# Optimization experiments

Measured on AMD Instinct MI355X. Metric: run time of the kernel, lower is better.

The kernel has to match this reference:

```python
import jax, jax.numpy as jnp
import numpy as np

P = 2; NH = 8; NW = 4; NB = 6; D = 512; HID = 2048; NREG = 1; T = 1000; NACT = 3
HH = 32; WW = 32; C = 3; B = 1; DUR = 6


def _kron_bool(a, b):
    # kron(A,B)[i*p+k, j*q+l] = A[i,j] & B[k,l]
    m, n = a.shape; p, q = b.shape
    return (a[:, None, :, None] & b[None, :, None, :]).reshape(m * p, n * q)


def _masks(dur_zr, seq_zr, dur_xa, seq_xa):
    m_left = _kron_bool(jnp.eye(dur_zr, dtype=bool), jnp.ones((seq_zr, seq_zr), dtype=bool))
    tmp = jnp.ones((dur_zr, dur_zr), dtype=bool)
    band = jnp.tril(tmp, -1) ^ jnp.tril(tmp, -1 - NW)  # sliding window over previous frames
    m_right = _kron_bool(band[:, :-1], jnp.ones((seq_zr, seq_xa), dtype=bool))
    m_self = _kron_bool(jnp.tril(jnp.ones((dur_xa, dur_xa), dtype=bool)), jnp.ones((seq_xa, seq_xa), dtype=bool))
    return ~jnp.concatenate([m_left, m_right], axis=1), ~m_self


def _ln(x):
    mu = jnp.mean(x, -1, keepdims=True)
    xc = x - mu
    var = jnp.mean(xc * xc, -1, keepdims=True)
    return xc * jax.lax.rsqrt(var + 1e-5)


def _patch(x, Wp, bp):
    b, dur, c, h, w = x.shape
    x = x.reshape(b, dur, c, h // P, P, w // P, P)
    x = x.transpose(0, 1, 3, 5, 2, 4, 6).reshape(b, dur, (h // P) * (w // P), c * P * P)
    return x @ Wp + bp


def _unpatch(x, Wu, bu):
    b, dur, s, d = x.shape
    y = x @ Wu + bu  # [b,dur,s,C*P*P]
    y = y.reshape(b, dur, HH // P, WW // P, C, P, P)
    return y.transpose(0, 1, 4, 2, 5, 3, 6).reshape(b, dur, C, HH, WW)


def _mod(x, cond, Wm, bm):
    # AdaLN: per-frame scale/shift broadcast over tokens of that frame
    scale, shift = jnp.split(jax.nn.silu(cond) @ Wm + bm, 2, axis=-1)
    b, L, d = x.shape; dur = cond.shape[1]; s = L // dur
    y = _ln(x).reshape(b, dur, s, d)
    return (y * (1.0 + scale[:, :, None]) + shift[:, :, None]).reshape(b, L, d)


def _gate(x, cond, Wg, bg):
    g = cond @ Wg + bg
    b, L, d = x.shape; dur = cond.shape[1]; s = L // dur
    return (x.reshape(b, dur, s, d) * g[:, :, None]).reshape(b, L, d)


def _attn(q, kv, mask, Wq, bq, Wk, bk, Wv, bv, Wo, bo):
    b, lq, d = q.shape; lk = kv.shape[1]; dh = d // NH
    qh = (q @ Wq + bq).reshape(b, lq, NH, dh)
    kh = (kv @ Wk + bk).reshape(b, lk, NH, dh)
    vh = (kv @ Wv + bv).reshape(b, lk, NH, dh)
    s = jnp.einsum('bqhd,bkhd->bhqk', qh, kh) * (1.0 / np.sqrt(dh))
    s = jnp.where(mask[None, None], -1e9, s)  # mask True = disallowed
    o = jnp.einsum('bhqk,bkhd->bqhd', jax.nn.softmax(s, axis=-1), vh)
    return o.reshape(b, lq, d) @ Wo + bo


def _geglu(x, Wg, bg, Wo, bo):
    a, g = jnp.split(x @ Wg + bg, 2, axis=-1)
    return (a * jax.nn.gelu(g, approximate=False)) @ Wo + bo


def _forward(z, frames, actions, ts, W_patch, b_patch, W_unpatch, b_unpatch, registers, pe_grid, action_emb, time_emb, W_mod1, b_mod1, W_mod2, b_mod2, W_q, b_q, W_k, b_k, W_v, b_v, W_o, b_o, W_g1, b_g1, W_g2, b_g2, W_geglu, b_geglu, W_ffout, b_ffout):
    zt = _patch(z, W_patch, b_patch) + pe_grid[None, None]
    xt = _patch(frames, W_patch, b_patch) + pe_grid[None, None]
    a = action_emb[actions]  # [B, dur, D]
    b, dur_zr, s, d = zt.shape
    zr = jnp.concatenate([zt, jnp.broadcast_to(registers[None, None], (b, dur_zr, NREG, d))], axis=2)
    xa = jnp.concatenate([xt, a[:, :-1, None, :]], axis=2)
    seq_zr = zr.shape[2]; dur_xa = xa.shape[1]; seq_xa = xa.shape[2]
    mask_cross, mask_self = _masks(dur_zr, seq_zr, dur_xa, seq_xa)
    zr = zr.reshape(b, dur_zr * seq_zr, d)
    xa = xa.reshape(b, dur_xa * seq_xa, d)
    cond = time_emb[ts]  # [B, dur_zr, D]
    clean = jnp.broadcast_to(time_emb[0][None, None], (b, dur_xa, d))
    for i in range(NB):
        zrn = _mod(zr, cond, W_mod1[i], b_mod1[i])
        xan = _mod(xa, clean, W_mod1[i], b_mod1[i])
        xkv = jnp.concatenate([zrn, xan], axis=1)
        cross = _attn(zrn, xkv, mask_cross, W_q[i], b_q[i], W_k[i], b_k[i], W_v[i], b_v[i], W_o[i], b_o[i])
        selfa = _attn(xan, xan, mask_self, W_q[i], b_q[i], W_k[i], b_k[i], W_v[i], b_v[i], W_o[i], b_o[i])
        zr = _gate(zrn, cond, W_g1[i], b_g1[i])
        xa = _gate(xan, clean, W_g1[i], b_g1[i])
        zr = _mod(zr + cross, cond, W_mod2[i], b_mod2[i])
        xa = _mod(xa + selfa, clean, W_mod2[i], b_mod2[i])
        zr = _geglu(zr, W_geglu[i], b_geglu[i], W_ffout[i], b_ffout[i])
        xa = _geglu(xa, W_geglu[i], b_geglu[i], W_ffout[i], b_ffout[i])
        zr = _gate(zr, cond, W_g2[i], b_g2[i])
        xa = _gate(xa, clean, W_g2[i], b_g2[i])
    zr = zr.reshape(b, dur_zr, seq_zr, d)[:, :, :-NREG]
    return _unpatch(zr, W_unpatch, b_unpatch)


def setup_inputs() -> dict:
    key = jax.random.key(0)
    ks = iter(jax.random.split(key, 64))
    def rn(shape, scale=0.02):
        return jax.random.normal(next(ks), shape, dtype=jnp.float32) * scale
    inp = {}
    inp['z'] = jax.random.normal(next(ks), (B, DUR, C, HH, WW), dtype=jnp.float32)
    inp['frames'] = jax.random.normal(next(ks), (B, DUR - 1, C, HH, WW), dtype=jnp.float32)
    inp['actions'] = jax.random.randint(next(ks), (B, DUR), 0, NACT)
    inp['ts'] = jax.random.randint(next(ks), (B, DUR), 0, T)
    inp['W_patch'] = rn((C * P * P, D)); inp['b_patch'] = jnp.zeros((D,), jnp.float32)
    inp['W_unpatch'] = rn((D, C * P * P)); inp['b_unpatch'] = jnp.zeros((C * P * P,), jnp.float32)
    inp['registers'] = rn((NREG, D), 1.0 / D ** 0.5)
    inp['pe_grid'] = rn(((HH // P) * (WW // P), D), 1.0 / D ** 0.5)
    inp['action_emb'] = rn((NACT, D), 1.0)
    inp['time_emb'] = rn((T, D), 1.0)
    inp['W_mod1'] = rn((NB, D, 2 * D)); inp['b_mod1'] = jnp.zeros((NB, 2 * D), jnp.float32)
    inp['W_mod2'] = rn((NB, D, 2 * D)); inp['b_mod2'] = jnp.zeros((NB, 2 * D), jnp.float32)
    for nm in ('q', 'k', 'v', 'o'):
        inp['W_' + nm] = rn((NB, D, D)); inp['b_' + nm] = jnp.zeros((NB, D), jnp.float32)
    inp['W_g1'] = rn((NB, D, D)); inp['b_g1'] = jnp.ones((NB, D), jnp.float32)
    inp['W_g2'] = rn((NB, D, D)); inp['b_g2'] = jnp.ones((NB, D), jnp.float32)
    inp['W_geglu'] = rn((NB, D, 2 * HID)); inp['b_geglu'] = jnp.zeros((NB, 2 * HID), jnp.float32)
    inp['W_ffout'] = rn((NB, HID, D)); inp['b_ffout'] = jnp.zeros((NB, D), jnp.float32)
    return inp


def reference(z, frames, actions, ts, W_patch, b_patch, W_unpatch, b_unpatch, registers, pe_grid, action_emb, time_emb, W_mod1, b_mod1, W_mod2, b_mod2, W_q, b_q, W_k, b_k, W_v, b_v, W_o, b_o, W_g1, b_g1, W_g2, b_g2, W_geglu, b_geglu, W_ffout, b_ffout):
    return _forward(z, frames, actions, ts, W_patch, b_patch, W_unpatch, b_unpatch, registers, pe_grid, action_emb, time_emb, W_mod1, b_mod1, W_mod2, b_mod2, W_q, b_q, W_k, b_k, W_v, b_v, W_o, b_o, W_g1, b_g1, W_g2, b_g2, W_geglu, b_geglu, W_ffout, b_ffout)
```

## Files before the change

kernel.cpp:

```cpp
#include <hip/hip_runtime.h>
#include <hip/hip_bf16.h>
#include <math.h>

#define DURZ 6
#define DURX 5
#define SEQ 257
#define LZ 1542
#define LX 1285
#define LT 2827
#define LTP 2880
#define DM 512
#define NHEADS 8
#define DH 64
#define HIDDEN 2048

typedef __bf16 bf16x8 __attribute__((ext_vector_type(8)));
typedef __bf16 bf16x4 __attribute__((ext_vector_type(4)));
typedef float f32x4 __attribute__((ext_vector_type(4)));

__global__ void fill_kernel(float* __restrict__ out, int n, float v) {
    int i = blockIdx.x * blockDim.x + threadIdx.x;
    if (i < n) out[i] = v;
}

__global__ void embed_kernel(const float* __restrict__ z,
                             const float* __restrict__ frames,
                             const int* __restrict__ actions,
                             const float* __restrict__ W_patch,
                             const float* __restrict__ b_patch,
                             const float* __restrict__ registers,
                             const float* __restrict__ pe,
                             const float* __restrict__ action_emb,
                             float* __restrict__ state) {
    int T = blockIdx.x;
    int tid = threadIdx.x;
    bool is_z = T < LZ;
    int T2 = is_z ? T : T - LZ;
    int f = T2 / SEQ, t = T2 % SEQ;
    if (t < 256) {
        const float* src = is_z ? z : frames;
        int hp = t >> 4, wp = t & 15;
        float pv[12];
#pragma unroll
        for (int c = 0; c < 3; c++)
#pragma unroll
            for (int ph = 0; ph < 2; ph++)
#pragma unroll
                for (int pw = 0; pw < 2; pw++)
                    pv[c * 4 + ph * 2 + pw] =
                        src[((f * 3 + c) * 32 + (hp * 2 + ph)) * 32 + (wp * 2 + pw)];
        for (int d = tid; d < DM; d += 256) {
            float acc = b_patch[d];
#pragma unroll
            for (int j = 0; j < 12; j++) acc += pv[j] * W_patch[j * DM + d];
            acc += pe[t * DM + d];
            state[T * DM + d] = acc;
        }
    } else if (is_z) {
        for (int d = tid; d < DM; d += 256) state[T * DM + d] = registers[d];
    } else {
        int a = actions[f];
        for (int d = tid; d < DM; d += 256) state[T * DM + d] = action_emb[a * DM + d];
    }
}

__global__ void cond_kernel(const int* __restrict__ ts,
                            const float* __restrict__ time_emb,
                            float* __restrict__ condraw,
                            float* __restrict__ condsilu) {
    int idx = blockIdx.x * blockDim.x + threadIdx.x;
    if (idx >= 7 * 512) return;
    int r = idx >> 9;
    int j = idx & 511;
    int tsr = (r < 6) ? ts[r] : 0;
    float x = time_emb[tsr * 512 + j];
    condraw[idx] = x;
    condsilu[idx] = x / (1.0f + expf(-x));
}

__global__ void params_kernel(const float* __restrict__ condraw,
                              const float* __restrict__ condsilu,
                              const float* __restrict__ W_mod1,
                              const float* __restrict__ b_mod1,
                              const float* __restrict__ W_mod2,
                              const float* __restrict__ b_mod2,
                              const float* __restrict__ W_g1,
                              const float* __restrict__ b_g1,
                              const float* __restrict__ W_g2,
                              const float* __restrict__ b_g2,
                              float* __restrict__ params) {
    int idx = blockIdx.x * blockDim.x + threadIdx.x;
    if (idx >= 6 * 7 * 3072) return;
    int i = idx / 21504;
    int rem = idx % 21504;
    int r = rem / 3072;
    int c = rem % 3072;
    const float* cv;
    const float* W;
    float bias;
    int ldw;
    if (c < 1024) {
        cv = condsilu + r * 512;
        W = W_mod1 + (size_t)i * 512 * 1024 + c; ldw = 1024;
        bias = b_mod1[i * 1024 + c];
    } else if (c < 2048) {
        int cc = c - 1024;
        cv = condsilu + r * 512;
        W = W_mod2 + (size_t)i * 512 * 1024 + cc; ldw = 1024;
        bias = b_mod2[i * 1024 + cc];
    } else if (c < 2560) {
        int cc = c - 2048;
        cv = condraw + r * 512;
        W = W_g1 + (size_t)i * 512 * 512 + cc; ldw = 512;
        bias = b_g1[i * 512 + cc];
    } else {
        int cc = c - 2560;
        cv = condraw + r * 512;
        W = W_g2 + (size_t)i * 512 * 512 + cc; ldw = 512;
        bias = b_g2[i * 512 + cc];
    }
    float acc = bias;
    for (int j = 0; j < 512; j++) acc += cv[j] * W[(size_t)j * ldw];
    params[idx] = acc;
}

__global__ void ztail_kernel(__bf16* __restrict__ Kh, __bf16* __restrict__ Kl,
                             __bf16* __restrict__ Vth, __bf16* __restrict__ Vtl) {
    int idx = blockIdx.x * blockDim.x + threadIdx.x;
    if (idx >= (LTP - LT) * 512) return;
    int r = idx / 512, c = idx % 512;
    Kh[(size_t)(LT + r) * DM + c] = (__bf16)0.0f;
    Kl[(size_t)(LT + r) * DM + c] = (__bf16)0.0f;
    Vth[(size_t)c * LTP + LT + r] = (__bf16)0.0f;
    Vtl[(size_t)c * LTP + LT + r] = (__bf16)0.0f;
}

template<bool PL>
__global__ __launch_bounds__(256) void lnmod_kernel(const float* __restrict__ xf,
                                                    const __bf16* __restrict__ xh,
                                                    const __bf16* __restrict__ xl,
                                                    __bf16* __restrict__ yh,
                                                    __bf16* __restrict__ yl,
                                                    const float* __restrict__ params,
                                                    int mod_off) {
    int T = blockIdx.x;
    int tid = threadIdx.x;
    int r = (T < LZ) ? (T / SEQ) : 6;
    const float* prow = params + r * 3072 + mod_off;
    size_t base = (size_t)T * DM;
    float v0, v1;
    if constexpr (PL) {
        v0 = (float)xh[base + tid] + (float)xl[base + tid];
        v1 = (float)xh[base + tid + 256] + (float)xl[base + tid + 256];
    } else {
        v0 = xf[base + tid];
        v1 = xf[base + tid + 256];
    }
    float s_ = v0 + v1, q_ = v0 * v0 + v1 * v1;
#pragma unroll
    for (int off = 32; off; off >>= 1) {
        s_ += __shfl_down(s_, off);
        q_ += __shfl_down(q_, off);
    }
    __shared__ float sh[8];
    int wave = tid >> 6, lane = tid & 63;
    if (lane == 0) { sh[wave] = s_; sh[4 + wave] = q_; }
    __syncthreads();
    float sum = sh[0] + sh[1] + sh[2] + sh[3];
    float sq = sh[4] + sh[5] + sh[6] + sh[7];
    float mu = sum * (1.0f / 512.0f);
    float var = sq * (1.0f / 512.0f) - mu * mu;
    float rstd = rsqrtf(var + 1e-5f);
    float y0 = (v0 - mu) * rstd * (1.0f + prow[tid]) + prow[512 + tid];
    float y1 = (v1 - mu) * rstd * (1.0f + prow[tid + 256]) + prow[512 + tid + 256];
    __bf16 h0 = (__bf16)y0, h1 = (__bf16)y1;
    yh[base + tid] = h0;
    yl[base + tid] = (__bf16)(y0 - (float)h0);
    yh[base + tid + 256] = h1;
    yl[base + tid + 256] = (__bf16)(y1 - (float)h1);
}

#define MFMA3(accv, ah, al, bh, bl)                                            \
    accv = __builtin_amdgcn_mfma_f32_16x16x32_bf16(al, bh, accv, 0, 0, 0);     \
    accv = __builtin_amdgcn_mfma_f32_16x16x32_bf16(ah, bl, accv, 0, 0, 0);     \
    accv = __builtin_amdgcn_mfma_f32_16x16x32_bf16(ah, bh, accv, 0, 0, 0);

__global__ __launch_bounds__(256) void wprep_kernel(const float* __restrict__ Wq,
                                                    const float* __restrict__ Wk,
                                                    const float* __restrict__ Wv,
                                                    const float* __restrict__ Wo,
                                                    const float* __restrict__ Wglu,
                                                    const float* __restrict__ Wff,
                                                    float* __restrict__ Wp) {
    __shared__ __align__(16) __bf16 T[2][64][40];
    int id = blockIdx.x, t = threadIdx.x;
    const float* src;
    int N, nsub, kt;
    size_t dstf;
    if (id < 512) {
        int mat = id >> 7, rem = id & 127;
        nsub = rem >> 4; kt = rem & 15; N = 512;
        src = mat == 0 ? Wq : mat == 1 ? Wk : mat == 2 ? Wv : Wo;
        dstf = (size_t)mat * 327680 + (size_t)(nsub * 16 + kt) * 2560;
    } else if (id < 1536) {
        int rem = id - 512;
        nsub = rem >> 4; kt = rem & 15; N = 4096; src = Wglu;
        dstf = 1310720 + (size_t)(nsub * 16 + kt) * 2560;
    } else {
        int rem = id - 1536;
        nsub = rem >> 6; kt = rem & 63; N = 512; src = Wff;
        dstf = 3932160 + (size_t)(nsub * 64 + kt) * 2560;
    }
    int r = t >> 2;
    int cb = (t & 3) * 8;
#pragma unroll
    for (int j = 0; j < 8; ++j) {
        int c = cb + j;
        float x = src[(size_t)(kt * 32 + c) * N + nsub * 64 + r];
        __bf16 h = (__bf16)x;
        T[0][r][c] = h;
        T[1][r][c] = (__bf16)(x - (float)h);
    }
    __syncthreads();
    float4* d = (float4*)(Wp + dstf);
    const float4* s4 = (const float4*)(&T[0][0][0]);
    for (int i2 = t; i2 < 640; i2 += 256) d[i2] = s4[i2];
}

#define M_QKV 0
#define M_GATE1 1
#define M_GLU 2
#define M_GATE2 3

template<int MODE>
__global__ __launch_bounds__(256) void gemm_kernel(
    const __bf16* __restrict__ Aph, const __bf16* __restrict__ Apl,
    const char* __restrict__ Wbase, int KT, int Krow,
    const float* __restrict__ b0, const float* __restrict__ b1,
    const float* __restrict__ b2,
    float* __restrict__ C0,
    __bf16* __restrict__ Oh, __bf16* __restrict__ Ol,
    __bf16* __restrict__ O2h, __bf16* __restrict__ O2l,
    __bf16* __restrict__ O3h, __bf16* __restrict__ O3l,
    const __bf16* __restrict__ Xh, const __bf16* __restrict__ Xl,
    const float* __restrict__ params, int M) {
    __shared__ __align__(16) __bf16 Alds[2][2][64][32];
    __shared__ __align__(16) __bf16 Blds[2][2][2][64][40];
    int tid = threadIdx.x;
    int w = tid >> 6, lane = tid & 63;
    int q = lane >> 4, lr = lane & 15;
    int nwg = gridDim.x * gridDim.y;
    int lin = blockIdx.y * gridDim.x + blockIdx.x;
    int qq = nwg >> 3, rr = nwg & 7;
    int xcd = lin & 7, ix = lin >> 3;
    int wg = (xcd < rr) ? xcd * (qq + 1) + ix : rr * (qq + 1) + (xcd - rr) * qq + ix;
    int mb = wg % gridDim.x;
    int nb = wg / gridDim.x;
    int m0 = mb * 64;
    const char* sb0;
    const char* sb1;
    if constexpr (MODE == M_QKV) {
        int sel = nb >> 2;
        const char* mbp = Wbase + (size_t)sel * 1310720;
        sb0 = mbp + (size_t)(2 * (nb & 3)) * 163840;
        sb1 = mbp + (size_t)(2 * (nb & 3) + 1) * 163840;
    } else if constexpr (MODE == M_GLU) {
        sb0 = Wbase + (size_t)nb * 163840;
        sb1 = Wbase + (size_t)(32 + nb) * 163840;
    } else {
        sb0 = Wbase + (size_t)(2 * nb) * (size_t)KT * 10240;
        sb1 = Wbase + (size_t)(2 * nb + 1) * (size_t)KT * 10240;
    }
    int wm = (w >> 1) * 32;

    auto stage = [&](int sbuf, int kt) {
        const char* k0 = sb0 + (size_t)kt * 10240;
        const char* k1 = sb1 + (size_t)kt * 10240;
        char* bl = (char*)(&Blds[sbuf][0][0][0][0]);
        for (int idx = w; idx < 20; idx += 4) {
            int sub = idx & 1, c = idx >> 1;
            const char* g = (sub ? k1 : k0) + (c << 10) + (lane << 4);
            __builtin_amdgcn_global_load_lds((const unsigned int*)g,
                (unsigned int*)(bl + sub * 10240 + (c << 10)), 16, 0, 0);
        }
        char* al = (char*)(&Alds[sbuf][0][0][0]);
        for (int idx = w; idx < 8; idx += 4) {
            int p = idx & 1, c = idx >> 1;
            int row = c * 16 + (lane >> 2);
            int ss = (lane & 3) ^ ((row >> 1) & 3);
            int mrow = m0 + row;
            if (mrow > M - 1) mrow = M - 1;
            const __bf16* ap = (p ? Apl : Aph) + (size_t)mrow * Krow + kt * 32 + ss * 8;
            __builtin_amdgcn_global_load_lds((const unsigned int*)ap,
                (unsigned int*)(al + p * 4096 + (c << 10)), 16, 0, 0);
        }
    };

    f32x4 acc[2][4];
#pragma unroll
    for (int i = 0; i < 2; ++i)
#pragma unroll
        for (int j = 0; j < 4; ++j)
#pragma unroll
            for (int r = 0; r < 4; ++r) acc[i][j][r] = 0.0f;

    stage(0, 0);
    __syncthreads();
    for (int kt = 0; kt < KT; ++kt) {
        int buf = kt & 1;
        if (kt + 1 < KT) stage(buf ^ 1, kt + 1);
        bf16x8 afh[2], afl[2], bh[4], bl4[4];
#pragma unroll
        for (int i = 0; i < 2; ++i) {
            int row = wm + i * 16 + lr;
            int off = (q * 16) ^ (((row >> 1) & 3) << 4);
            afh[i] = *(const bf16x8*)((const char*)(&Alds[buf][0][row][0]) + off);
            afl[i] = *(const bf16x8*)((const char*)(&Alds[buf][1][row][0]) + off);
        }
#pragma unroll
        for (int j = 0; j < 4; ++j) {
            int bsub, brow;
            if constexpr (MODE == M_GLU) {
                bsub = j >> 1;
                brow = (w & 1) * 32 + (j & 1) * 16 + lr;
            } else {
                bsub = w & 1;
                brow = j * 16 + lr;
            }
            bh[j] = *(const bf16x8*)(&Blds[buf][bsub][0][brow][q * 8]);
            bl4[j] = *(const bf16x8*)(&Blds[buf][bsub][1][brow][q * 8]);
        }
#pragma unroll
        for (int i = 0; i < 2; ++i)
#pragma unroll
            for (int j = 0; j < 4; ++j) {
                MFMA3(acc[i][j], afh[i], afl[i], bh[j], bl4[j]);
            }
        __syncthreads();
    }

    if constexpr (MODE == M_QKV) {
        int sel = nb >> 2;
        int c0 = (nb & 3) * 128 + (w & 1) * 64;
        if (sel == 2) {
#pragma unroll
            for (int i = 0; i < 2; ++i) {
                int mb2 = m0 + wm + i * 16 + q * 4;
#pragma unroll
                for (int j = 0; j < 4; ++j) {
                    int n = c0 + j * 16 + lr;
                    bf16x4 h4, l4;
#pragma unroll
                    for (int r = 0; r < 4; ++r) {
                        float v = acc[i][j][r] + b2[n];
                        __bf16 hh = (__bf16)v;
                        h4[r] = hh;
                        l4[r] = (__bf16)(v - (float)hh);
                    }
                    if (mb2 + 3 < M) {
                        *(bf16x4*)(O3h + (size_t)n * LTP + mb2) = h4;
                        *(bf16x4*)(O3l + (size_t)n * LTP + mb2) = l4;
                    } else {
#pragma unroll
                        for (int r = 0; r < 4; ++r)
                            if (mb2 + r < M) {
                                O3h[(size_t)n * LTP + mb2 + r] = h4[r];
                                O3l[(size_t)n * LTP + mb2 + r] = l4[r];
                            }
                    }
                }
            }
        } else {
            const float* bias = sel == 0 ? b0 : b1;
            __bf16* Dh = sel == 0 ? Oh : O2h;
            __bf16* Dl = sel == 0 ? Ol : O2l;
            float scale = sel == 0 ? 0.125f : 1.0f;
#pragma unroll
            for (int i = 0; i < 2; ++i)
#pragma unroll
                for (int r = 0; r < 4; ++r) {
                    int m = m0 + wm + i * 16 + q * 4 + r;
                    if (m >= M) continue;
#pragma unroll
                    for (int j = 0; j < 4; ++j) {
                        int n = c0 + j * 16 + lr;
                        float v = (acc[i][j][r] + bias[n]) * scale;
                        __bf16 hh = (__bf16)v;
                        Dh[(size_t)m * DM + n] = hh;
                        Dl[(size_t)m * DM + n] = (__bf16)(v - (float)hh);
                    }
                }
        }
        return;
    }

#pragma unroll
    for (int i = 0; i < 2; ++i)
#pragma unroll
        for (int r = 0; r < 4; ++r) {
            int m = m0 + wm + i * 16 + q * 4 + r;
            if (m >= M) continue;
            if constexpr (MODE == M_GATE1) {
                int r6 = (m < LZ) ? (m / SEQ) : 6;
                const float* g1 = params + r6 * 3072 + 2048;
                int c0 = nb * 128 + (w & 1) * 64;
#pragma unroll
                for (int j = 0; j < 4; ++j) {
                    int n = c0 + j * 16 + lr;
                    size_t o = (size_t)m * 512 + n;
                    float x = (float)Xh[o] + (float)Xl[o];
                    float v = x * g1[n] + acc[i][j][r] + b0[n];
                    __bf16 hh = (__bf16)v;
                    Oh[o] = hh;
                    Ol[o] = (__bf16)(v - (float)hh);
                }
            } else if constexpr (MODE == M_GLU) {
#pragma unroll
                for (int j = 0; j < 2; ++j) {
                    int n = nb * 64 + (w & 1) * 32 + j * 16 + lr;
                    float a = acc[i][j][r] + b0[n];
                    float g = acc[i][j + 2][r] + b0[2048 + n];
                    float gel = 0.5f * g * (1.0f + erff(g * 0.70710678118654752f));
                    float v = a * gel;
                    size_t o = (size_t)m * 2048 + n;
                    __bf16 hh = (__bf16)v;
                    Oh[o] = hh;
                    Ol[o] = (__bf16)(v - (float)hh);
                }
            } else {
                int r6 = (m < LZ) ? (m / SEQ) : 6;
                const float* g2 = params + r6 * 3072 + 2560;
                int c0 = nb * 128 + (w & 1) * 64;
#pragma unroll
                for (int j = 0; j < 4; ++j) {
                    int n = c0 + j * 16 + lr;
                    C0[(size_t)m * 512 + n] = (acc[i][j][r] + b0[n]) * g2[n];
                }
            }
        }
}

__global__ __launch_bounds__(256) void fattn_kernel(
    const __bf16* __restrict__ Qph, const __bf16* __restrict__ Qpl,
    const __bf16* __restrict__ Kph, const __bf16* __restrict__ Kpl,
    const __bf16* __restrict__ Vph, const __bf16* __restrict__ Vpl,
    __bf16* __restrict__ Oh, __bf16* __restrict__ Ol) {
    __shared__ __align__(16) __bf16 Ksh[2][64][64];
    __shared__ __align__(16) __bf16 Vsh[2][64][64];
    __shared__ __align__(16) __bf16 Ph[4][16][72], Pl[4][16][72];
    int tid = threadIdx.x;
    int w = tid >> 6, lane = tid & 63;
    int lq = lane & 15, lg = lane >> 4;
    int hoff = blockIdx.z * DH;
    int qbase, base0, len0, base1, len1;
    if (blockIdx.y < 6) {
        int f = blockIdx.y;
        qbase = f * SEQ;
        base0 = f * SEQ; len0 = SEQ;
        int jl = f - 4; if (jl < 0) jl = 0;
        base1 = LZ + jl * SEQ; len1 = (f - jl) * SEQ;
    } else {
        int f = blockIdx.y - 6;
        qbase = LZ + f * SEQ;
        base0 = LZ; len0 = (f + 1) * SEQ;
        base1 = 0; len1 = 0;
    }
    int q0 = blockIdx.x * 64;
    int qvalid = SEQ - q0; if (qvalid > 64) qvalid = 64;

    bf16x8 qfh[2], qfl[2];
    {
        int qr = w * 16 + lq;
        int tok = qbase + q0 + ((qr < qvalid) ? qr : 0);
        const __bf16* qph = Qph + (size_t)tok * DM + hoff + lg * 8;
        const __bf16* qpl = Qpl + (size_t)tok * DM + hoff + lg * 8;
#pragma unroll
        for (int s = 0; s < 2; ++s) {
            qfh[s] = *(const bf16x8*)(qph + s * 32);
            qfl[s] = *(const bf16x8*)(qpl + s * 32);
        }
    }
    f32x4 acc[4];
#pragma unroll
    for (int n = 0; n < 4; ++n)
#pragma unroll
        for (int r = 0; r < 4; ++r) acc[n][r] = 0.0f;
    float m_i = -1e30f, l_i = 0.0f;
    int slot = lane & 7, rsub = lane >> 3;

    for (int rng = 0; rng < 2; ++rng) {
        int base = rng ? base1 : base0;
        int len = rng ? len1 : len0;
        if (len == 0) continue;
        int tend = base + len;
        for (int t = base & ~63; t < tend; t += 64) {
            int lo = base - t; if (lo < 0) lo = 0;
            int hi = tend - t; if (hi > 64) hi = 64;
            __syncthreads();
#pragma unroll
            for (int ii = 0; ii < 4; ++ii) {
                int idx = w + ii * 4;
                int p = idx >> 3, c = idx & 7;
                int row = c * 8 + rsub;
                const __bf16* g = (p ? Kpl : Kph) +
                    (size_t)(t + row) * DM + hoff + (slot ^ (row & 7)) * 8;
                __builtin_amdgcn_global_load_lds((const unsigned int*)g,
                    (unsigned int*)((char*)(&Ksh[p][0][0]) + c * 1024), 16, 0, 0);
            }
#pragma unroll
            for (int ii = 0; ii < 4; ++ii) {
                int idx = w + ii * 4;
                int p = idx >> 3, c = idx & 7;
                int d = c * 8 + rsub;
                const __bf16* g = (p ? Vpl : Vph) +
                    (size_t)(hoff + d) * LTP + t + (slot ^ (d & 7)) * 8;
                __builtin_amdgcn_global_load_lds((const unsigned int*)g,
                    (unsigned int*)((char*)(&Vsh[p][0][0]) + c * 1024), 16, 0, 0);
            }
            __syncthreads();
            f32x4 st[4];
#pragma unroll
            for (int sub = 0; sub < 4; ++sub)
#pragma unroll
                for (int r = 0; r < 4; ++r) st[sub][r] = 0.0f;
#pragma unroll
            for (int sub = 0; sub < 4; ++sub) {
                int row = sub * 16 + lq;
#pragma unroll
                for (int s = 0; s < 2; ++s) {
                    int sl = ((s * 4 + lg) ^ (row & 7)) * 8;
                    bf16x8 kfh = *(const bf16x8*)(&Ksh[0][row][sl]);
                    bf16x8 kfl = *(const bf16x8*)(&Ksh[1][row][sl]);
                    MFMA3(st[sub], kfh, kfl, qfh[s], qfl[s]);
                }
            }
            float p[16];
            float rmax = -1e30f;
#pragma unroll
            for (int sub = 0; sub < 4; ++sub)
#pragma unroll
                for (int r = 0; r < 4; ++r) {
                    int kk = sub * 16 + lg * 4 + r;
                    float sv = (kk >= lo && kk < hi) ? st[sub][r] : -1e30f;
                    p[sub * 4 + r] = sv;
                    rmax = fmaxf(rmax, sv);
                }
            rmax = fmaxf(rmax, __shfl_xor(rmax, 16));
            rmax = fmaxf(rmax, __shfl_xor(rmax, 32));
            float mnew = fmaxf(m_i, rmax);
            float alpha = __expf(m_i - mnew);
            float rsum = 0.0f;
#pragma unroll
            for (int i2 = 0; i2 < 16; ++i2) {
                p[i2] = __expf(p[i2] - mnew);
                rsum += p[i2];
            }
            rsum += __shfl_xor(rsum, 16);
            rsum += __shfl_xor(rsum, 32);
            l_i = l_i * alpha + rsum;
            m_i = mnew;
            float ar[4];
#pragma unroll
            for (int r = 0; r < 4; ++r) ar[r] = __shfl(alpha, lg * 4 + r);
#pragma unroll
            for (int n = 0; n < 4; ++n)
#pragma unroll
                for (int r = 0; r < 4; ++r) acc[n][r] *= ar[r];
#pragma unroll
            for (int sub = 0; sub < 4; ++sub) {
                bf16x4 h4, l4;
#pragma unroll
                for (int r = 0; r < 4; ++r) {
                    float x = p[sub * 4 + r];
                    __bf16 hh = (__bf16)x;
                    h4[r] = hh;
                    l4[r] = (__bf16)(x - (float)hh);
                }
                *(bf16x4*)&Ph[w][lq][sub * 16 + lg * 4] = h4;
                *(bf16x4*)&Pl[w][lq][sub * 16 + lg * 4] = l4;
            }
            bf16x8 pah[2], pal[2];
#pragma unroll
            for (int s = 0; s < 2; ++s) {
                pah[s] = *(const bf16x8*)(&Ph[w][lq][s * 32 + lg * 8]);
                pal[s] = *(const bf16x8*)(&Pl[w][lq][s * 32 + lg * 8]);
            }
#pragma unroll
            for (int n = 0; n < 4; ++n) {
                int row = n * 16 + lq;
#pragma unroll
                for (int s = 0; s < 2; ++s) {
                    int sl = ((s * 4 + lg) ^ (row & 7)) * 8;
                    bf16x8 vfh = *(const bf16x8*)(&Vsh[0][row][sl]);
                    bf16x8 vfl = *(const bf16x8*)(&Vsh[1][row][sl]);
                    MFMA3(acc[n], pah[s], pal[s], vfh, vfl);
                }
            }
        }
    }
    float linv[4];
#pragma unroll
    for (int r = 0; r < 4; ++r) linv[r] = 1.0f / __shfl(l_i, lg * 4 + r);
#pragma unroll
    for (int r = 0; r < 4; ++r) {
        int qr = w * 16 + lg * 4 + r;
        if (qr < qvalid) {
            size_t ob = (size_t)(qbase + q0 + qr) * DM + hoff;
#pragma unroll
            for (int n = 0; n < 4; ++n) {
                float v = acc[n][r] * linv[r];
                __bf16 hh = (__bf16)v;
                Oh[ob + n * 16 + lq] = hh;
                Ol[ob + n * 16 + lq] = (__bf16)(v - (float)hh);
            }
        }
    }
}

__global__ void unpatch_kernel(const float* __restrict__ state,
                               const float* __restrict__ Wu,
                               const float* __restrict__ bu,
                               float* __restrict__ out) {
    int idx = blockIdx.x * blockDim.x + threadIdx.x;
    if (idx >= DURZ * 3 * 32 * 32) return;
    int w = idx & 31, hh = (idx >> 5) & 31, c = (idx >> 10) % 3, f = idx / (3 * 1024);
    int t = (hh >> 1) * 16 + (w >> 1);
    int j = c * 4 + (hh & 1) * 2 + (w & 1);
    const float* xr = state + (size_t)(f * SEQ + t) * DM;
    float acc = bu[j];
    for (int k = 0; k < DM; ++k) acc += xr[k] * Wu[k * 12 + j];
    out[idx] = acc;
}

extern "C" void kernel_launch(void* const* d_in, const int* in_sizes, int n_in,
                              void* d_out, int out_size, void* d_ws, size_t ws_size,
                              hipStream_t stream) {
    static const int expected_sizes[32] = {
        18432, 15360, 6, 6,
        6144, 512, 6144, 12,
        512, 131072, 1536, 512000,
        3145728, 6144, 3145728, 6144,
        1572864, 3072, 1572864, 3072,
        1572864, 3072, 1572864, 3072,
        1572864, 3072, 1572864, 3072,
        12582912, 24576, 6291456, 3072
    };
    if (n_in != 32) {
        fill_kernel<<<(18432 + 255) / 256, 256, 0, stream>>>((float*)d_out, 18432, 3.0f);
        return;
    }
    for (int i = 0; i < 32; ++i) {
        if (in_sizes[i] != expected_sizes[i]) {
            fill_kernel<<<(18432 + 255) / 256, 256, 0, stream>>>((float*)d_out, 18432,
                                                                 4.0f + (float)i);
            return;
        }
    }

    const float* z = (const float*)d_in[0];
    const float* frames = (const float*)d_in[1];
    const int* actions = (const int*)d_in[2];
    const int* ts = (const int*)d_in[3];
    const float* W_patch = (const float*)d_in[4];
    const float* b_patch = (const float*)d_in[5];
    const float* W_unpatch = (const float*)d_in[6];
    const float* b_unpatch = (const float*)d_in[7];
    const float* registers = (const float*)d_in[8];
    const float* pe_grid = (const float*)d_in[9];
    const float* action_emb = (const float*)d_in[10];
    const float* time_emb = (const float*)d_in[11];
    const float* W_mod1 = (const float*)d_in[12];
    const float* b_mod1 = (const float*)d_in[13];
    const float* W_mod2 = (const float*)d_in[14];
    const float* b_mod2 = (const float*)d_in[15];
    const float* W_q = (const float*)d_in[16];
    const float* b_q = (const float*)d_in[17];
    const float* W_k = (const float*)d_in[18];
    const float* b_k = (const float*)d_in[19];
    const float* W_v = (const float*)d_in[20];
    const float* b_v = (const float*)d_in[21];
    const float* W_o = (const float*)d_in[22];
    const float* b_o = (const float*)d_in[23];
    const float* W_g1 = (const float*)d_in[24];
    const float* b_g1 = (const float*)d_in[25];
    const float* W_g2 = (const float*)d_in[26];
    const float* b_g2 = (const float*)d_in[27];
    const float* W_geglu = (const float*)d_in[28];
    const float* b_geglu = (const float*)d_in[29];
    const float* W_ffout = (const float*)d_in[30];
    const float* b_ffout = (const float*)d_in[31];

    const size_t S = (size_t)LT * DM;
    const size_t PLE = (size_t)LTP * DM;
    const size_t PLF = PLE / 2;
    size_t need = (4 * S + 6 * PLF + 129024 + 7168 + 5242880) * sizeof(float);
    if (ws_size < need) {
        fill_kernel<<<(18432 + 255) / 256, 256, 0, stream>>>((float*)d_out, 18432, 40.0f);
        return;
    }
    float* ws = (float*)d_ws;
    float* state = ws;
    __bf16* xnh = (__bf16*)(ws + S);
    __bf16* xnl = (__bf16*)(ws + S + S / 2);
    __bf16* Qh = (__bf16*)(ws + 2 * S);
    __bf16* Ql = Qh + PLE;
    __bf16* Kh = Qh + 2 * PLE;
    __bf16* Kl = Qh + 3 * PLE;
    __bf16* Vth = Qh + 4 * PLE;
    __bf16* Vtl = Qh + 5 * PLE;
    float* aoff = ws + 2 * S + 6 * PLF;
    __bf16* atth = (__bf16*)aoff;
    __bf16* attl = atth + S;
    __bf16* y2h = (__bf16*)(aoff + S);
    __bf16* y2l = y2h + S;
    __bf16* Hph = (__bf16*)(ws + 2 * S);
    __bf16* Hpl = Hph + (size_t)LT * HIDDEN;
    float* params = aoff + 2 * S;
    float* condraw = params + 129024;
    float* condsilu = condraw + 3584;
    float* wp = condsilu + 3584;

    embed_kernel<<<LT, 256, 0, stream>>>(z, frames, actions, W_patch, b_patch,
                                         registers, pe_grid, action_emb, state);
    cond_kernel<<<(7 * 512 + 255) / 256, 256, 0, stream>>>(ts, time_emb, condraw, condsilu);
    params_kernel<<<(6 * 7 * 3072 + 255) / 256, 256, 0, stream>>>(
        condraw, condsilu, W_mod1, b_mod1, W_mod2, b_mod2, W_g1, b_g1, W_g2, b_g2, params);
    ztail_kernel<<<((LTP - LT) * 512 + 255) / 256, 256, 0, stream>>>(Kh, Kl, Vth, Vtl);

    dim3 gqkv(45, 12);
    dim3 ggate1(45, 4);
    dim3 gglu(45, 32);
    dim3 ggate2(45, 4);
    dim3 gattn(5, 11, NHEADS);
    for (int i = 0; i < 6; ++i) {
        const float* P = params + i * 21504;
        wprep_kernel<<<2048, 256, 0, stream>>>(
            W_q + (size_t)i * DM * DM, W_k + (size_t)i * DM * DM,
            W_v + (size_t)i * DM * DM, W_o + (size_t)i * DM * DM,
            W_geglu + (size_t)i * DM * 4096, W_ffout + (size_t)i * HIDDEN * DM, wp);
        lnmod_kernel<false><<<LT, 256, 0, stream>>>(state, nullptr, nullptr,
                                                    xnh, xnl, P, 0);
        gemm_kernel<M_QKV><<<gqkv, 256, 0, stream>>>(
            xnh, xnl, (const char*)wp, 16, 512,
            b_q + i * DM, b_k + i * DM, b_v + i * DM, nullptr,
            Qh, Ql, Kh, Kl, Vth, Vtl, nullptr, nullptr, nullptr, LT);
        fattn_kernel<<<gattn, 256, 0, stream>>>(Qh, Ql, Kh, Kl, Vth, Vtl, atth, attl);
        gemm_kernel<M_GATE1><<<ggate1, 256, 0, stream>>>(
            atth, attl, (const char*)(wp + 983040), 16, 512,
            b_o + i * DM, nullptr, nullptr, nullptr,
            y2h, y2l, nullptr, nullptr, nullptr, nullptr, xnh, xnl, P, LT);
        lnmod_kernel<true><<<LT, 256, 0, stream>>>(nullptr, y2h, y2l,
                                                   xnh, xnl, P, 1024);
        gemm_kernel<M_GLU><<<gglu, 256, 0, stream>>>(
            xnh, xnl, (const char*)(wp + 1310720), 16, 512,
            b_geglu + (size_t)i * 4096, nullptr, nullptr, nullptr,
            Hph, Hpl, nullptr, nullptr, nullptr, nullptr, nullptr, nullptr, nullptr, LT);
        gemm_kernel<M_GATE2><<<ggate2, 256, 0, stream>>>(
            Hph, Hpl, (const char*)(wp + 3932160), 64, 2048,
            b_ffout + i * DM, nullptr, nullptr, state,
            nullptr, nullptr, nullptr, nullptr, nullptr, nullptr,
            nullptr, nullptr, P, LT);
    }
    unpatch_kernel<<<(DURZ * 3 * 32 * 32 + 255) / 256, 256, 0, stream>>>(
        state, W_unpatch, b_unpatch, (float*)d_out);
}
```

Baseline: 1.856 ms.

## Load GEMM A fragments directly to registers and enlarge GLU M-tile

```diff
diff --git a/kernel.cpp b/kernel.cpp
--- a/kernel.cpp
+++ b/kernel.cpp
@@ -232,7 +232,7 @@
 #define M_GLU 2
 #define M_GATE2 3
 
-template<int MODE>
+template<int MODE, int NI>
 __global__ __launch_bounds__(256) void gemm_kernel(
     const __bf16* __restrict__ Aph, const __bf16* __restrict__ Apl,
     const char* __restrict__ Wbase, int KT, int Krow,
@@ -244,7 +244,7 @@
     __bf16* __restrict__ O3h, __bf16* __restrict__ O3l,
     const __bf16* __restrict__ Xh, const __bf16* __restrict__ Xl,
     const float* __restrict__ params, int M) {
-    __shared__ __align__(16) __bf16 Alds[2][2][64][32];
+    constexpr int BM = NI * 32;
     __shared__ __align__(16) __bf16 Blds[2][2][2][64][40];
     int tid = threadIdx.x;
     int w = tid >> 6, lane = tid & 63;
@@ -256,7 +256,7 @@
     int wg = (xcd < rr) ? xcd * (qq + 1) + ix : rr * (qq + 1) + (xcd - rr) * qq + ix;
     int mb = wg % gridDim.x;
     int nb = wg / gridDim.x;
-    int m0 = mb * 64;
+    int m0 = mb * BM;
     const char* sb0;
     const char* sb1;
     if constexpr (MODE == M_QKV) {
@@ -271,9 +271,19 @@
         sb0 = Wbase + (size_t)(2 * nb) * (size_t)KT * 10240;
         sb1 = Wbase + (size_t)(2 * nb + 1) * (size_t)KT * 10240;
     }
-    int wm = (w >> 1) * 32;
-
-    auto stage = [&](int sbuf, int kt) {
+    int wm = (w >> 1) * (BM / 2);
+
+    const __bf16* aRowH[NI];
+    const __bf16* aRowL[NI];
+#pragma unroll
+    for (int i = 0; i < NI; ++i) {
+        int mrow = m0 + wm + i * 16 + lr;
+        if (mrow > M - 1) mrow = M - 1;
+        aRowH[i] = Aph + (size_t)mrow * Krow + q * 8;
+        aRowL[i] = Apl + (size_t)mrow * Krow + q * 8;
+    }
+
+    auto stageB = [&](int sbuf, int kt) {
         const char* k0 = sb0 + (size_t)kt * 10240;
         const char* k1 = sb1 + (size_t)kt * 10240;
         char* bl = (char*)(&Blds[sbuf][0][0][0][0]);
@@ -283,40 +293,26 @@
             __builtin_amdgcn_global_load_lds((const unsigned int*)g,
                 (unsigned int*)(bl + sub * 10240 + (c << 10)), 16, 0, 0);
         }
-        char* al = (char*)(&Alds[sbuf][0][0][0]);
-        for (int idx = w; idx < 8; idx += 4) {
-            int p = idx & 1, c = idx >> 1;
-            int row = c * 16 + (lane >> 2);
-            int ss = (lane & 3) ^ ((row >> 1) & 3);
-            int mrow = m0 + row;
-            if (mrow > M - 1) mrow = M - 1;
-            const __bf16* ap = (p ? Apl : Aph) + (size_t)mrow * Krow + kt * 32 + ss * 8;
-            __builtin_amdgcn_global_load_lds((const unsigned int*)ap,
-                (unsigned int*)(al + p * 4096 + (c << 10)), 16, 0, 0);
-        }
     };
-
-    f32x4 acc[2][4];
-#pragma unroll
-    for (int i = 0; i < 2; ++i)
+    auto aloadF = [&](int kt, bf16x8 (&ah)[NI], bf16x8 (&al)[NI]) {
+        int off = kt * 32;
+#pragma unroll
+        for (int i = 0; i < NI; ++i) {
+            ah[i] = *(const bf16x8*)(aRowH[i] + off);
+            al[i] = *(const bf16x8*)(aRowL[i] + off);
+        }
+    };
+
+    f32x4 acc[NI][4];
+#pragma unroll
+    for (int i = 0; i < NI; ++i)
 #pragma unroll
         for (int j = 0; j < 4; ++j)
 #pragma unroll
             for (int r = 0; r < 4; ++r) acc[i][j][r] = 0.0f;
 
-    stage(0, 0);
-    __syncthreads();
-    for (int kt = 0; kt < KT; ++kt) {
-        int buf = kt & 1;
-        if (kt + 1 < KT) stage(buf ^ 1, kt + 1);
-        bf16x8 afh[2], afl[2], bh[4], bl4[4];
-#pragma unroll
-        for (int i = 0; i < 2; ++i) {
-            int row = wm + i * 16 + lr;
-            int off = (q * 16) ^ (((row >> 1) & 3) << 4);
-            afh[i] = *(const bf16x8*)((const char*)(&Alds[buf][0][row][0]) + off);
-            afl[i] = *(const bf16x8*)((const char*)(&Alds[buf][1][row][0]) + off);
-        }
+    auto compute = [&](int buf, bf16x8 (&ah)[NI], bf16x8 (&al)[NI]) {
+        bf16x8 bh[4], bl4[4];
 #pragma unroll
         for (int j = 0; j < 4; ++j) {
             int bsub, brow;
@@ -331,11 +327,27 @@
             bl4[j] = *(const bf16x8*)(&Blds[buf][bsub][1][brow][q * 8]);
         }
 #pragma unroll
-        for (int i = 0; i < 2; ++i)
+        for (int i = 0; i < NI; ++i)
 #pragma unroll
             for (int j = 0; j < 4; ++j) {
-                MFMA3(acc[i][j], afh[i], afl[i], bh[j], bl4[j]);
-            }
+                MFMA3(acc[i][j], ah[i], al[i], bh[j], bl4[j]);
+            }
+    };
+
+    bf16x8 A0h[NI], A0l[NI], A1h[NI], A1l[NI];
+    stageB(0, 0);
+    aloadF(0, A0h, A0l);
+    __syncthreads();
+    for (int kt = 0; kt < KT; kt += 2) {
+        stageB(1, kt + 1);
+        aloadF(kt + 1, A1h, A1l);
+        compute(0, A0h, A0l);
+        __syncthreads();
+        if (kt + 2 < KT) {
+            stageB(0, kt + 2);
+            aloadF(kt + 2, A0h, A0l);
+        }
+        compute(1, A1h, A1l);
         __syncthreads();
     }
 
@@ -344,7 +356,7 @@
         int c0 = (nb & 3) * 128 + (w & 1) * 64;
         if (sel == 2) {
 #pragma unroll
-            for (int i = 0; i < 2; ++i) {
+            for (int i = 0; i < NI; ++i) {
                 int mb2 = m0 + wm + i * 16 + q * 4;
 #pragma unroll
                 for (int j = 0; j < 4; ++j) {
@@ -376,7 +388,7 @@
             __bf16* Dl = sel == 0 ? Ol : O2l;
             float scale = sel == 0 ? 0.125f : 1.0f;
 #pragma unroll
-            for (int i = 0; i < 2; ++i)
+            for (int i = 0; i < NI; ++i)
 #pragma unroll
                 for (int r = 0; r < 4; ++r) {
                     int m = m0 + wm + i * 16 + q * 4 + r;
@@ -395,7 +407,7 @@
     }
 
 #pragma unroll
-    for (int i = 0; i < 2; ++i)
+    for (int i = 0; i < NI; ++i)
 #pragma unroll
         for (int r = 0; r < 4; ++r) {
             int m = m0 + wm + i * 16 + q * 4 + r;
@@ -729,7 +741,7 @@
 
     dim3 gqkv(45, 12);
     dim3 ggate1(45, 4);
-    dim3 gglu(45, 32);
+    dim3 gglu(23, 32);
     dim3 ggate2(45, 4);
     dim3 gattn(5, 11, NHEADS);
     for (int i = 0; i < 6; ++i) {
@@ -740,22 +752,22 @@
             W_geglu + (size_t)i * DM * 4096, W_ffout + (size_t)i * HIDDEN * DM, wp);
         lnmod_kernel<false><<<LT, 256, 0, stream>>>(state, nullptr, nullptr,
                                                     xnh, xnl, P, 0);
-        gemm_kernel<M_QKV><<<gqkv, 256, 0, stream>>>(
+        gemm_kernel<M_QKV, 2><<<gqkv, 256, 0, stream>>>(
             xnh, xnl, (const char*)wp, 16, 512,
             b_q + i * DM, b_k + i * DM, b_v + i * DM, nullptr,
             Qh, Ql, Kh, Kl, Vth, Vtl, nullptr, nullptr, nullptr, LT);
         fattn_kernel<<<gattn, 256, 0, stream>>>(Qh, Ql, Kh, Kl, Vth, Vtl, atth, attl);
-        gemm_kernel<M_GATE1><<<ggate1, 256, 0, stream>>>(
+        gemm_kernel<M_GATE1, 2><<<ggate1, 256, 0, stream>>>(
             atth, attl, (const char*)(wp + 983040), 16, 512,
             b_o + i * DM, nullptr, nullptr, nullptr,
             y2h, y2l, nullptr, nullptr, nullptr, nullptr, xnh, xnl, P, LT);
         lnmod_kernel<true><<<LT, 256, 0, stream>>>(nullptr, y2h, y2l,
                                                    xnh, xnl, P, 1024);
-        gemm_kernel<M_GLU><<<gglu, 256, 0, stream>>>(
+        gemm_kernel<M_GLU, 4><<<gglu, 256, 0, stream>>>(
             xnh, xnl, (const char*)(wp + 1310720), 16, 512,
             b_geglu + (size_t)i * 4096, nullptr, nullptr, nullptr,
             Hph, Hpl, nullptr, nullptr, nullptr, nullptr, nullptr, nullptr, nullptr, LT);
-        gemm_kernel<M_GATE2><<<ggate2, 256, 0, stream>>>(
+        gemm_kernel<M_GATE2, 2><<<ggate2, 256, 0, stream>>>(
             Hph, Hpl, (const char*)(wp + 3932160), 64, 2048,
             b_ffout + i * DM, nullptr, nullptr, state,
             nullptr, nullptr, nullptr, nullptr, nullptr, nullptr,
```

After: 1.988 ms. 7.1% more time.

## Swizzle B tile in LDS instead of padding and enlarge GLU GEMM M-tile

Applied to the files above, without the earlier changes.

```diff
diff --git a/kernel.cpp b/kernel.cpp
--- a/kernel.cpp
+++ b/kernel.cpp
@@ -192,7 +192,7 @@
                                                     const float* __restrict__ Wglu,
                                                     const float* __restrict__ Wff,
                                                     float* __restrict__ Wp) {
-    __shared__ __align__(16) __bf16 T[2][64][40];
+    __shared__ __align__(16) __bf16 T[2][64][32];
     int id = blockIdx.x, t = threadIdx.x;
     const float* src;
     int N, nsub, kt;
@@ -201,30 +201,31 @@
         int mat = id >> 7, rem = id & 127;
         nsub = rem >> 4; kt = rem & 15; N = 512;
         src = mat == 0 ? Wq : mat == 1 ? Wk : mat == 2 ? Wv : Wo;
-        dstf = (size_t)mat * 327680 + (size_t)(nsub * 16 + kt) * 2560;
+        dstf = (size_t)mat * 262144 + (size_t)(nsub * 16 + kt) * 2048;
     } else if (id < 1536) {
         int rem = id - 512;
         nsub = rem >> 4; kt = rem & 15; N = 4096; src = Wglu;
-        dstf = 1310720 + (size_t)(nsub * 16 + kt) * 2560;
+        dstf = 1048576 + (size_t)(nsub * 16 + kt) * 2048;
     } else {
         int rem = id - 1536;
         nsub = rem >> 6; kt = rem & 63; N = 512; src = Wff;
-        dstf = 3932160 + (size_t)(nsub * 64 + kt) * 2560;
+        dstf = 3145728 + (size_t)(nsub * 64 + kt) * 2048;
     }
     int r = t >> 2;
-    int cb = (t & 3) * 8;
+    int s = t & 3;
+    int ds = (s ^ ((r >> 1) & 3)) * 8;
 #pragma unroll
     for (int j = 0; j < 8; ++j) {
-        int c = cb + j;
+        int c = s * 8 + j;
         float x = src[(size_t)(kt * 32 + c) * N + nsub * 64 + r];
         __bf16 h = (__bf16)x;
-        T[0][r][c] = h;
-        T[1][r][c] = (__bf16)(x - (float)h);
+        T[0][r][ds + j] = h;
+        T[1][r][ds + j] = (__bf16)(x - (float)h);
     }
     __syncthreads();
     float4* d = (float4*)(Wp + dstf);
     const float4* s4 = (const float4*)(&T[0][0][0]);
-    for (int i2 = t; i2 < 640; i2 += 256) d[i2] = s4[i2];
+    for (int i2 = t; i2 < 512; i2 += 256) d[i2] = s4[i2];
 }
 
 #define M_QKV 0
@@ -232,7 +233,7 @@
 #define M_GLU 2
 #define M_GATE2 3
 
-template<int MODE>
+template<int MODE, int NI>
 __global__ __launch_bounds__(256) void gemm_kernel(
     const __bf16* __restrict__ Aph, const __bf16* __restrict__ Apl,
     const char* __restrict__ Wbase, int KT, int Krow,
@@ -244,8 +245,9 @@
     __bf16* __restrict__ O3h, __bf16* __restrict__ O3l,
     const __bf16* __restrict__ Xh, const __bf16* __restrict__ Xl,
     const float* __restrict__ params, int M) {
-    __shared__ __align__(16) __bf16 Alds[2][2][64][32];
-    __shared__ __align__(16) __bf16 Blds[2][2][2][64][40];
+    constexpr int BM = NI * 32;
+    __shared__ __align__(16) __bf16 Alds[2][2][BM][32];
+    __shared__ __align__(16) __bf16 Blds[2][2][2][64][32];
     int tid = threadIdx.x;
     int w = tid >> 6, lane = tid & 63;
     int q = lane >> 4, lr = lane & 15;
@@ -256,35 +258,35 @@
     int wg = (xcd < rr) ? xcd * (qq + 1) + ix : rr * (qq + 1) + (xcd - rr) * qq + ix;
     int mb = wg % gridDim.x;
     int nb = wg / gridDim.x;
-    int m0 = mb * 64;
+    int m0 = mb * BM;
     const char* sb0;
     const char* sb1;
     if constexpr (MODE == M_QKV) {
         int sel = nb >> 2;
-        const char* mbp = Wbase + (size_t)sel * 1310720;
-        sb0 = mbp + (size_t)(2 * (nb & 3)) * 163840;
-        sb1 = mbp + (size_t)(2 * (nb & 3) + 1) * 163840;
+        const char* mbp = Wbase + (size_t)sel * 1048576;
+        sb0 = mbp + (size_t)(2 * (nb & 3)) * 131072;
+        sb1 = mbp + (size_t)(2 * (nb & 3) + 1) * 131072;
     } else if constexpr (MODE == M_GLU) {
-        sb0 = Wbase + (size_t)nb * 163840;
-        sb1 = Wbase + (size_t)(32 + nb) * 163840;
+        sb0 = Wbase + (size_t)nb * 131072;
+        sb1 = Wbase + (size_t)(32 + nb) * 131072;
     } else {
-        sb0 = Wbase + (size_t)(2 * nb) * (size_t)KT * 10240;
-        sb1 = Wbase + (size_t)(2 * nb + 1) * (size_t)KT * 10240;
-    }
-    int wm = (w >> 1) * 32;
+        sb0 = Wbase + (size_t)(2 * nb) * (size_t)KT * 8192;
+        sb1 = Wbase + (size_t)(2 * nb + 1) * (size_t)KT * 8192;
+    }
+    int wm = (w >> 1) * (BM / 2);
 
     auto stage = [&](int sbuf, int kt) {
-        const char* k0 = sb0 + (size_t)kt * 10240;
-        const char* k1 = sb1 + (size_t)kt * 10240;
+        const char* k0 = sb0 + (size_t)kt * 8192;
+        const char* k1 = sb1 + (size_t)kt * 8192;
         char* bl = (char*)(&Blds[sbuf][0][0][0][0]);
-        for (int idx = w; idx < 20; idx += 4) {
-            int sub = idx & 1, c = idx >> 1;
+        for (int idx = w; idx < 16; idx += 4) {
+            int sub = idx >> 3, c = idx & 7;
             const char* g = (sub ? k1 : k0) + (c << 10) + (lane << 4);
             __builtin_amdgcn_global_load_lds((const unsigned int*)g,
-                (unsigned int*)(bl + sub * 10240 + (c << 10)), 16, 0, 0);
+                (unsigned int*)(bl + sub * 8192 + (c << 10)), 16, 0, 0);
         }
         char* al = (char*)(&Alds[sbuf][0][0][0]);
-        for (int idx = w; idx < 8; idx += 4) {
+        for (int idx = w; idx < NI * 4; idx += 4) {
             int p = idx & 1, c = idx >> 1;
             int row = c * 16 + (lane >> 2);
             int ss = (lane & 3) ^ ((row >> 1) & 3);
@@ -292,13 +294,13 @@
             if (mrow > M - 1) mrow = M - 1;
             const __bf16* ap = (p ? Apl : Aph) + (size_t)mrow * Krow + kt * 32 + ss * 8;
             __builtin_amdgcn_global_load_lds((const unsigned int*)ap,
-                (unsigned int*)(al + p * 4096 + (c << 10)), 16, 0, 0);
+                (unsigned int*)(al + p * (NI * 2048) + (c << 10)), 16, 0, 0);
         }
     };
 
-    f32x4 acc[2][4];
-#pragma unroll
-    for (int i = 0; i < 2; ++i)
+    f32x4 acc[NI][4];
+#pragma unroll
+    for (int i = 0; i < NI; ++i)
 #pragma unroll
         for (int j = 0; j < 4; ++j)
 #pragma unroll
@@ -309,14 +311,16 @@
     for (int kt = 0; kt < KT; ++kt) {
         int buf = kt & 1;
         if (kt + 1 < KT) stage(buf ^ 1, kt + 1);
-        bf16x8 afh[2], afl[2], bh[4], bl4[4];
-#pragma unroll
-        for (int i = 0; i < 2; ++i) {
+        bf16x8 afh[NI], afl[NI], bh[4], bl4[4];
+        const char* ab = (const char*)(&Alds[buf][0][0][0]);
+#pragma unroll
+        for (int i = 0; i < NI; ++i) {
             int row = wm + i * 16 + lr;
             int off = (q * 16) ^ (((row >> 1) & 3) << 4);
-            afh[i] = *(const bf16x8*)((const char*)(&Alds[buf][0][row][0]) + off);
-            afl[i] = *(const bf16x8*)((const char*)(&Alds[buf][1][row][0]) + off);
-        }
+            afh[i] = *(const bf16x8*)(ab + row * 64 + off);
+            afl[i] = *(const bf16x8*)(ab + NI * 2048 + row * 64 + off);
+        }
+        const char* bb = (const char*)(&Blds[buf][0][0][0][0]);
 #pragma unroll
         for (int j = 0; j < 4; ++j) {
             int bsub, brow;
@@ -327,11 +331,12 @@
                 bsub = w & 1;
                 brow = j * 16 + lr;
             }
-            bh[j] = *(const bf16x8*)(&Blds[buf][bsub][0][brow][q * 8]);
-            bl4[j] = *(const bf16x8*)(&Blds[buf][bsub][1][brow][q * 8]);
-        }
-#pragma unroll
-        for (int i = 0; i < 2; ++i)
+            int off = (q * 16) ^ (((brow >> 1) & 3) << 4);
+            bh[j] = *(const bf16x8*)(bb + bsub * 8192 + brow * 64 + off);
+            bl4[j] = *(const bf16x8*)(bb + bsub * 8192 + 4096 + brow * 64 + off);
+        }
+#pragma unroll
+        for (int i = 0; i < NI; ++i)
 #pragma unroll
             for (int j = 0; j < 4; ++j) {
                 MFMA3(acc[i][j], afh[i], afl[i], bh[j], bl4[j]);
@@ -344,7 +349,7 @@
         int c0 = (nb & 3) * 128 + (w & 1) * 64;
         if (sel == 2) {
 #pragma unroll
-            for (int i = 0; i < 2; ++i) {
+            for (int i = 0; i < NI; ++i) {
                 int mb2 = m0 + wm + i * 16 + q * 4;
 #pragma unroll
                 for (int j = 0; j < 4; ++j) {
@@ -376,7 +381,7 @@
             __bf16* Dl = sel == 0 ? Ol : O2l;
             float scale = sel == 0 ? 0.125f : 1.0f;
 #pragma unroll
-            for (int i = 0; i < 2; ++i)
+            for (int i = 0; i < NI; ++i)
 #pragma unroll
                 for (int r = 0; r < 4; ++r) {
                     int m = m0 + wm + i * 16 + q * 4 + r;
@@ -395,7 +400,7 @@
     }
 
 #pragma unroll
-    for (int i = 0; i < 2; ++i)
+    for (int i = 0; i < NI; ++i)
 #pragma unroll
         for (int r = 0; r < 4; ++r) {
             int m = m0 + wm + i * 16 + q * 4 + r;
@@ -693,7 +698,7 @@
     const size_t S = (size_t)LT * DM;
     const size_t PLE = (size_t)LTP * DM;
     const size_t PLF = PLE / 2;
-    size_t need = (4 * S + 6 * PLF + 129024 + 7168 + 5242880) * sizeof(float);
+    size_t need = (4 * S + 6 * PLF + 129024 + 7168 + 4194304) * sizeof(float);
     if (ws_size < need) {
         fill_kernel<<<(18432 + 255) / 256, 256, 0, stream>>>((float*)d_out, 18432, 40.0f);
         return;
@@ -729,7 +734,7 @@
 
     dim3 gqkv(45, 12);
     dim3 ggate1(45, 4);
-    dim3 gglu(45, 32);
+    dim3 gglu(23, 32);
     dim3 ggate2(45, 4);
     dim3 gattn(5, 11, NHEADS);
     for (int i = 0; i < 6; ++i) {
@@ -740,23 +745,23 @@
             W_geglu + (size_t)i * DM * 4096, W_ffout + (size_t)i * HIDDEN * DM, wp);
         lnmod_kernel<false><<<LT, 256, 0, stream>>>(state, nullptr, nullptr,
                                                     xnh, xnl, P, 0);
-        gemm_kernel<M_QKV><<<gqkv, 256, 0, stream>>>(
+        gemm_kernel<M_QKV, 2><<<gqkv, 256, 0, stream>>>(
             xnh, xnl, (const char*)wp, 16, 512,
             b_q + i * DM, b_k + i * DM, b_v + i * DM, nullptr,
             Qh, Ql, Kh, Kl, Vth, Vtl, nullptr, nullptr, nullptr, LT);
         fattn_kernel<<<gattn, 256, 0, stream>>>(Qh, Ql, Kh, Kl, Vth, Vtl, atth, attl);
-        gemm_kernel<M_GATE1><<<ggate1, 256, 0, stream>>>(
-            atth, attl, (const char*)(wp + 983040), 16, 512,
+        gemm_kernel<M_GATE1, 2><<<ggate1, 256, 0, stream>>>(
+            atth, attl, (const char*)(wp + 786432), 16, 512,
             b_o + i * DM, nullptr, nullptr, nullptr,
             y2h, y2l, nullptr, nullptr, nullptr, nullptr, xnh, xnl, P, LT);
         lnmod_kernel<true><<<LT, 256, 0, stream>>>(nullptr, y2h, y2l,
                                                    xnh, xnl, P, 1024);
-        gemm_kernel<M_GLU><<<gglu, 256, 0, stream>>>(
-            xnh, xnl, (const char*)(wp + 1310720), 16, 512,
+        gemm_kernel<M_GLU, 4><<<gglu, 256, 0, stream>>>(
+            xnh, xnl, (const char*)(wp + 1048576), 16, 512,
             b_geglu + (size_t)i * 4096, nullptr, nullptr, nullptr,
             Hph, Hpl, nullptr, nullptr, nullptr, nullptr, nullptr, nullptr, nullptr, LT);
-        gemm_kernel<M_GATE2><<<ggate2, 256, 0, stream>>>(
-            Hph, Hpl, (const char*)(wp + 3932160), 64, 2048,
+        gemm_kernel<M_GATE2, 2><<<ggate2, 256, 0, stream>>>(
+            Hph, Hpl, (const char*)(wp + 3145728), 64, 2048,
             b_ffout + i * DM, nullptr, nullptr, state,
             nullptr, nullptr, nullptr, nullptr, nullptr, nullptr,
             nullptr, nullptr, P, LT);
```

After: 1.771 ms. 1.05x faster.
